# Kernel tuning notes

Hardware: AMD Instinct MI355X
Metric: run time of the kernel (lower is better)

## Reference

```python
import jax, jax.numpy as jnp
import numpy as np

WIN = 7          # window height/width
P = 10           # prompts_len
HEADS = 12
B0 = 32          # image batch (spa_prompts batch)
NW = 64          # windows per image
NW_TOK = WIN * WIN  # 49


def _relative_position_index(w):
    coords = np.stack(np.meshgrid(np.arange(w), np.arange(w), indexing='ij'))  # [2,w,w]
    flat = coords.reshape(2, -1)                        # [2, w*w]
    rel = flat[:, :, None] - flat[:, None, :]           # [2, w*w, w*w]
    rel = rel.transpose(1, 2, 0).astype(np.int64)       # [w*w, w*w, 2]
    rel[..., 0] += w - 1
    rel[..., 1] += w - 1
    rel[..., 0] *= 2 * w - 1
    return rel.sum(-1)                                  # [w*w, w*w]

REL_IDX = jnp.asarray(_relative_position_index(WIN))    # [49,49] int


def setup_inputs() -> dict:
    key = jax.random.key(0)
    ks = jax.random.split(key, 8)
    dim = 384
    return {
        'x': jax.random.normal(ks[0], (B0 * NW, NW_TOK, dim), jnp.float32),
        'spa_prompts': jax.random.normal(ks[1], (B0, P, dim), jnp.float32),
        'mask': jax.random.normal(ks[2], (NW, NW_TOK, NW_TOK), jnp.float32),
        'bias_table': jax.random.normal(ks[3], (169, HEADS), jnp.float32) * 0.02,
        'w_qkv': jax.random.normal(ks[4], (3 * dim, dim), jnp.float32) * 0.02,
        'b_qkv': jax.random.normal(ks[5], (3 * dim,), jnp.float32) * 0.02,
        'w_proj': jax.random.normal(ks[6], (dim, dim), jnp.float32) * 0.02,
        'b_proj': jax.random.normal(ks[7], (dim,), jnp.float32) * 0.02,
    }


def reference(x, spa_prompts, mask, bias_table, w_qkv, b_qkv, w_proj, b_proj):
    B_, Nw, C = x.shape
    b0 = spa_prompts.shape[0]
    nW = B_ // b0
    hd = C // HEADS
    scale = hd ** -0.5

    # broadcast prompts to every window and prepend
    prompts = jnp.broadcast_to(spa_prompts[:, None], (b0, nW, P, C)).reshape(B_, P, C)
    xc = jnp.concatenate([prompts, x], axis=1)          # [B_, N, C], N = P + Nw
    N = xc.shape[1]

    qkv = xc @ w_qkv.T + b_qkv                          # [B_, N, 3C]
    qkv = qkv.reshape(B_, N, 3, HEADS, hd).transpose(2, 0, 3, 1, 4)
    q, k, v = qkv[0], qkv[1], qkv[2]                    # [B_, H, N, hd]

    attn_weight = jnp.einsum('bhnd,bhmd->bhnm', q, k)   # unscaled, returned

    # relative position bias gathered for the window block, padded over prompt rows/cols
    rpb = bias_table[REL_IDX.reshape(-1)].reshape(NW_TOK, NW_TOK, HEADS)
    rpb = rpb.transpose(2, 0, 1)                        # [H, 49, 49]
    bias_full = jnp.pad(rpb, ((0, 0), (P, 0), (P, 0)))  # [H, N, N]

    attn = attn_weight * scale + bias_full[None]

    mask_full = jnp.pad(mask, ((0, 0), (P, 0), (P, 0)))  # [nW, N, N]
    attn = attn.reshape(b0, nW, HEADS, N, N) + mask_full[None, :, None]
    attn = jax.nn.softmax(attn.reshape(B_, HEADS, N, N), axis=-1)

    out = jnp.einsum('bhnm,bhmd->bnhd', attn, v).reshape(B_, N, C)
    out = out @ w_proj.T + b_proj

    prompts_out = out[:, :P].reshape(b0, nW, P, C).mean(axis=1)
    x_out = out[:, P:]
    return (x_out, attn_weight, prompts_out)
```

## Files before the change

kernel.cpp:

```cpp
#include <hip/hip_runtime.h>
#include <hip/hip_bf16.h>

#define P     10
#define NTOK  59
#define HEADS 12
#define NWTOK 49

#define AW_OFF 38535168
#define PO_OFF 124096512

typedef __attribute__((ext_vector_type(8))) short short8;
typedef __attribute__((ext_vector_type(8))) unsigned short ushort8;
typedef __attribute__((ext_vector_type(4))) float floatx4;
typedef float f4u __attribute__((ext_vector_type(4), aligned(4)));
typedef unsigned int uint_g __attribute__((address_space(1)));
typedef unsigned int uint_l __attribute__((address_space(3)));

__device__ __forceinline__ unsigned short f2b(float f) {
  unsigned u = __builtin_bit_cast(unsigned, f);
  u += 0x7fffu + ((u >> 16) & 1u);
  return (unsigned short)(u >> 16);
}

__device__ __forceinline__ void gll16(const void* g, void* l) {
  __builtin_amdgcn_global_load_lds((const uint_g*)g, (uint_l*)l, 16, 0, 0);
}

__global__ __launch_bounds__(256) void convert_w_kernel(
    const float* __restrict__ w, unsigned short* __restrict__ wb) {
  const int i = (blockIdx.x * 256 + threadIdx.x) * 8;
  const float4 a = *(const float4*)(w + i);
  const float4 b = *(const float4*)(w + i + 4);
  ushort8 o;
  o[0] = f2b(a.x); o[1] = f2b(a.y); o[2] = f2b(a.z); o[3] = f2b(a.w);
  o[4] = f2b(b.x); o[5] = f2b(b.y); o[6] = f2b(b.z); o[7] = f2b(b.w);
  *(ushort8*)(wb + i) = o;
}

__global__ __launch_bounds__(256) void combo_kernel(
    const float* __restrict__ mask, const float* __restrict__ bias_table,
    float* __restrict__ combo) {
  const int bid = blockIdx.x;
  const int h = bid % HEADS, wnd = bid / HEADS;
  for (int e = threadIdx.x; e < 2401; e += 256) {
    const int ti = e / 49, tj = e - (e / 49) * 49;
    const int ai = ti / 7, aj = ti - ai * 7;
    const int bi = tj / 7, bj = tj - bi * 7;
    const int ridx = (ai - bi + 6) * 13 + (aj - bj + 6);
    combo[(size_t)bid * 2401 + e] =
        bias_table[ridx * HEADS + h] + mask[(size_t)wnd * 2401 + e];
  }
}

__global__ __launch_bounds__(256) void gemm_qkv_kernel(
    const unsigned short* __restrict__ xb, const unsigned short* __restrict__ xp,
    const unsigned short* __restrict__ Bw, const float* __restrict__ b_qkv,
    unsigned short* __restrict__ qkx, unsigned short* __restrict__ qkp) {
  __shared__ unsigned short Asw[8192];
  __shared__ unsigned short Bsw[8192];
  const int t = threadIdx.x;
  const int w = t >> 6, lane = t & 63;
  const int lr = lane & 15, lg = lane >> 4;
  const int w0 = w >> 1, w1 = w & 1;
  const int by = blockIdx.y;
  const bool isP = by >= 784;
  const int n0 = blockIdx.x * 128;
  const int srow = lane >> 3, cpos = lane & 7;

  floatx4 acc[4][4];
#pragma unroll
  for (int mr = 0; mr < 4; ++mr)
#pragma unroll
    for (int nc = 0; nc < 4; ++nc) acc[mr][nc] = (floatx4)0.f;

  for (int k0 = 0; k0 < 384; k0 += 64) {
#pragma unroll
    for (int i = 0; i < 4; ++i) {
      const int r = (w * 4 + i) * 8 + srow;
      const int c = cpos ^ (r & 7);
      const unsigned short* asrc;
      if (!isP) {
        asrc = xb + (size_t)(by * 128 + r) * 384 + k0 + c * 8;
      } else {
        int mp = (by - 784) * 128 + r;
        if (mp > 319) mp = 319;
        asrc = xp + (size_t)mp * 384 + k0 + c * 8;
      }
      gll16(asrc, Asw + (w * 4 + i) * 512);
      gll16(Bw + (size_t)(n0 + r) * 384 + k0 + c * 8, Bsw + (w * 4 + i) * 512);
    }
    __syncthreads();
#pragma unroll
    for (int kh = 0; kh < 2; ++kh) {
      short8 af[4], bf[4];
#pragma unroll
      for (int mr = 0; mr < 4; ++mr) {
        const int r = w0 * 64 + mr * 16 + lr;
        af[mr] = *(const short8*)(Asw + r * 64 + (((kh * 4 + lg) ^ (r & 7)) * 8));
      }
#pragma unroll
      for (int nc = 0; nc < 4; ++nc) {
        const int r = w1 * 64 + nc * 16 + lr;
        bf[nc] = *(const short8*)(Bsw + r * 64 + (((kh * 4 + lg) ^ (r & 7)) * 8));
      }
#pragma unroll
      for (int mr = 0; mr < 4; ++mr)
#pragma unroll
        for (int nc = 0; nc < 4; ++nc)
          acc[mr][nc] = __builtin_amdgcn_mfma_f32_16x16x32_bf16(
              af[mr], bf[nc], acc[mr][nc], 0, 0, 0);
    }
    __syncthreads();
  }

  const int sec = blockIdx.x / 3;
  float bias[4]; int hh[4], dd[4];
#pragma unroll
  for (int nc = 0; nc < 4; ++nc) {
    const int n = n0 + w1 * 64 + nc * 16 + lr;
    bias[nc] = b_qkv[n];
    hh[nc] = (n >> 5) % 12;
    dd[nc] = n & 31;
  }
#pragma unroll
  for (int mr = 0; mr < 4; ++mr)
#pragma unroll
    for (int reg = 0; reg < 4; ++reg) {
      const int rloc = w0 * 64 + mr * 16 + lg * 4 + reg;
      if (!isP) {
        const int m = by * 128 + rloc;
        const int bb = m / 49, tok = m - bb * 49;
        const size_t base = (size_t)(bb * 3 + sec) * 12 * 1568 + (size_t)tok * 32;
#pragma unroll
        for (int nc = 0; nc < 4; ++nc)
          qkx[base + (size_t)hh[nc] * 1568 + dd[nc]] =
              f2b(acc[mr][nc][reg] + bias[nc]);
      } else {
        const int mp = (by - 784) * 128 + rloc;
        if (mp < 320) {
          const int b0 = mp / 10, ptok = mp - b0 * 10;
          const size_t base = (size_t)(b0 * 3 + sec) * 12 * 320 + (size_t)ptok * 32;
#pragma unroll
          for (int nc = 0; nc < 4; ++nc)
            qkp[base + (size_t)hh[nc] * 320 + dd[nc]] =
                f2b(acc[mr][nc][reg] + bias[nc]);
        }
      }
    }
}

__global__ __launch_bounds__(256) void attn_kernel(
    const unsigned short* __restrict__ qkx, const unsigned short* __restrict__ qkp,
    const float* __restrict__ combo, float* __restrict__ aw_out,
    unsigned short* __restrict__ attn_bf) {
  __shared__ char lds[14976];
  unsigned short* qs = (unsigned short*)(lds);
  unsigned short* ks = (unsigned short*)(lds + 5120);
  unsigned short* vt = (unsigned short*)(lds + 10240);
  unsigned short* Pm = (unsigned short*)(lds);

  const int blk = blockIdx.x;
  const int b = blk / HEADS, h = blk - b * HEADS;
  const int t = threadIdx.x;
  const int w = t >> 6, lane = t & 63, lr = lane & 15, lg = lane >> 4;

  if (t < 236) {
    const int row = t >> 2, dc = (t & 3) * 8;
    ushort8 q8, k8, v8;
    if (row < P) {
      const size_t base =
          ((size_t)((b >> 6) * 3) * 12 + h) * 320 + row * 32 + dc;
      q8 = *(const ushort8*)(qkp + base);
      k8 = *(const ushort8*)(qkp + base + 12 * 320);
      v8 = *(const ushort8*)(qkp + base + 24 * 320);
    } else {
      const size_t base =
          ((size_t)(b * 3) * 12 + h) * 1568 + (row - P) * 32 + dc;
      q8 = *(const ushort8*)(qkx + base);
      k8 = *(const ushort8*)(qkx + base + 12 * 1568);
      v8 = *(const ushort8*)(qkx + base + 24 * 1568);
    }
    *(ushort8*)(qs + row * 40 + dc) = q8;
    *(ushort8*)(ks + row * 40 + dc) = k8;
#pragma unroll
    for (int j = 0; j < 8; ++j) vt[(dc + j) * 74 + row] = v8[j];
  } else {
    const int e = t - 236;
#pragma unroll
    for (int jj = 0; jj < 8; ++jj) {
      const int f = e * 8 + jj;
      vt[(f / 5) * 74 + 59 + (f % 5)] = 0;
    }
  }
  __syncthreads();

  const int q = w * 16 + lr;
  const short8 qa = *(const short8*)(qs + q * 40 + lg * 8);
  floatx4 sacc[4];
#pragma unroll
  for (int nt = 0; nt < 4; ++nt) {
    const short8 kb = *(const short8*)(ks + (nt * 16 + lr) * 40 + lg * 8);
    sacc[nt] = __builtin_amdgcn_mfma_f32_16x16x32_bf16(kb, qa, (floatx4)0.f, 0, 0, 0);
  }

  if (q < NTOK) {
    float* rowp = aw_out + (size_t)blk * 3481 + q * 59;
#pragma unroll
    for (int nt = 0; nt < 3; ++nt)
      *(f4u*)(rowp + nt * 16 + lg * 4) = __builtin_bit_cast(f4u, sacc[nt]);
    if (lg < 2) {
      *(f4u*)(rowp + 48 + lg * 4) = __builtin_bit_cast(f4u, sacc[3]);
    } else if (lg == 2) {
      rowp[56] = sacc[3][0];
      rowp[57] = sacc[3][1];
      rowp[58] = sacc[3][2];
    }
  }

  const float scale = 0.17677669529663687f;
  const float* comb = combo + (size_t)((b & 63) * HEADS + h) * 2401;
  float ev[4][4];
  float mx = -3.0e38f;
#pragma unroll
  for (int nt = 0; nt < 4; ++nt)
#pragma unroll
    for (int reg = 0; reg < 4; ++reg) {
      const int kk = nt * 16 + lg * 4 + reg;
      float v = -3.0e38f;
      if (q < NTOK && kk < NTOK) {
        const float cb = (q >= P && kk >= P) ? comb[(q - P) * 49 + (kk - P)] : 0.f;
        v = fmaf(sacc[nt][reg], scale, cb);
      }
      ev[nt][reg] = v;
      mx = fmaxf(mx, v);
    }
  mx = fmaxf(mx, __shfl_xor(mx, 16));
  mx = fmaxf(mx, __shfl_xor(mx, 32));
  float sm = 0.f;
#pragma unroll
  for (int nt = 0; nt < 4; ++nt)
#pragma unroll
    for (int reg = 0; reg < 4; ++reg) {
      const float e = __expf(ev[nt][reg] - mx);
      ev[nt][reg] = e;
      sm += e;
    }
  sm += __shfl_xor(sm, 16);
  sm += __shfl_xor(sm, 32);
  const float inv = 1.0f / sm;

  __syncthreads();
#pragma unroll
  for (int nt = 0; nt < 4; ++nt) {
    uint2 uu;
    uu.x = (unsigned)f2b(ev[nt][0] * inv) | ((unsigned)f2b(ev[nt][1] * inv) << 16);
    uu.y = (unsigned)f2b(ev[nt][2] * inv) | ((unsigned)f2b(ev[nt][3] * inv) << 16);
    *(uint2*)(Pm + q * 72 + nt * 16 + lg * 4) = uu;
  }

  floatx4 oacc[2];
  oacc[0] = (floatx4)0.f; oacc[1] = (floatx4)0.f;
#pragma unroll
  for (int kk = 0; kk < 2; ++kk) {
    const short8 pa = *(const short8*)(Pm + (w * 16 + lr) * 72 + kk * 32 + lg * 8);
#pragma unroll
    for (int nt = 0; nt < 2; ++nt) {
      const short8 vb = *(const short8*)(vt + (nt * 16 + lr) * 74 + kk * 32 + lg * 8);
      oacc[nt] = __builtin_amdgcn_mfma_f32_16x16x32_bf16(pa, vb, oacc[nt], 0, 0, 0);
    }
  }

  unsigned short* wb = Pm + w * 1152;
#pragma unroll
  for (int nt = 0; nt < 2; ++nt)
#pragma unroll
    for (int reg = 0; reg < 4; ++reg)
      wb[(lg * 4 + reg) * 40 + nt * 16 + lr] = f2b(oacc[nt][reg]);
  const int rr = lane >> 2, c8 = (lane & 3) * 8;
  const int row = w * 16 + rr;
  if (row < NTOK) {
    const ushort8 ov = *(const ushort8*)(wb + rr * 40 + c8);
    *(ushort8*)(attn_bf + ((size_t)(b * NTOK + row)) * 384 + h * 32 + c8) = ov;
  }
}

__global__ __launch_bounds__(256) void gemm_proj_kernel(
    const unsigned short* __restrict__ A, const unsigned short* __restrict__ Bw,
    const float* __restrict__ b_proj, float* __restrict__ x_out,
    float* __restrict__ pbuf) {
  __shared__ unsigned short Asw[8192];
  __shared__ unsigned short Bsw[8192];
  const int t = threadIdx.x;
  const int w = t >> 6, lane = t & 63;
  const int lr = lane & 15, lg = lane >> 4;
  const int w0 = w >> 1, w1 = w & 1;
  const size_t m0 = (size_t)blockIdx.y * 128;
  const int n0 = blockIdx.x * 128;
  const int srow = lane >> 3, cpos = lane & 7;

  floatx4 acc[4][4];
#pragma unroll
  for (int mr = 0; mr < 4; ++mr)
#pragma unroll
    for (int nc = 0; nc < 4; ++nc) acc[mr][nc] = (floatx4)0.f;

  for (int k0 = 0; k0 < 384; k0 += 64) {
#pragma unroll
    for (int i = 0; i < 4; ++i) {
      const int r = (w * 4 + i) * 8 + srow;
      const int c = cpos ^ (r & 7);
      gll16(A + (m0 + r) * 384 + k0 + c * 8, Asw + (w * 4 + i) * 512);
      gll16(Bw + (size_t)(n0 + r) * 384 + k0 + c * 8, Bsw + (w * 4 + i) * 512);
    }
    __syncthreads();
#pragma unroll
    for (int kh = 0; kh < 2; ++kh) {
      short8 af[4], bf[4];
#pragma unroll
      for (int mr = 0; mr < 4; ++mr) {
        const int r = w0 * 64 + mr * 16 + lr;
        af[mr] = *(const short8*)(Asw + r * 64 + (((kh * 4 + lg) ^ (r & 7)) * 8));
      }
#pragma unroll
      for (int nc = 0; nc < 4; ++nc) {
        const int r = w1 * 64 + nc * 16 + lr;
        bf[nc] = *(const short8*)(Bsw + r * 64 + (((kh * 4 + lg) ^ (r & 7)) * 8));
      }
#pragma unroll
      for (int mr = 0; mr < 4; ++mr)
#pragma unroll
        for (int nc = 0; nc < 4; ++nc)
          acc[mr][nc] = __builtin_amdgcn_mfma_f32_16x16x32_bf16(
              af[mr], bf[nc], acc[mr][nc], 0, 0, 0);
    }
    __syncthreads();
  }

  float bias[4]; int nn[4];
#pragma unroll
  for (int nc = 0; nc < 4; ++nc) {
    nn[nc] = n0 + w1 * 64 + nc * 16 + lr;
    bias[nc] = b_proj[nn[nc]];
  }
#pragma unroll
  for (int mr = 0; mr < 4; ++mr)
#pragma unroll
    for (int reg = 0; reg < 4; ++reg) {
      const int m = (int)m0 + w0 * 64 + mr * 16 + lg * 4 + reg;
      const int bb = m / 59, tok = m - bb * 59;
      float* dst = (tok >= P)
          ? x_out + (size_t)(bb * NWTOK + tok - P) * 384
          : pbuf + (size_t)(bb * P + tok) * 384;
#pragma unroll
      for (int nc = 0; nc < 4; ++nc)
        dst[nn[nc]] = acc[mr][nc][reg] + bias[nc];
    }
}

__global__ __launch_bounds__(256) void reduce_prompts_kernel(
    const float* __restrict__ pbuf, float* __restrict__ po) {
  const int o = blockIdx.x * 256 + threadIdx.x;
  const int b0 = o / 3840;
  const int rem = o - b0 * 3840;
  const float* base = pbuf + (size_t)b0 * 64 * 3840 + rem;
  float s = 0.f;
#pragma unroll 8
  for (int w = 0; w < 64; ++w) s += base[(size_t)w * 3840];
  po[o] = s * (1.f / 64.f);
}

extern "C" void kernel_launch(void* const* d_in, const int* in_sizes, int n_in,
                              void* d_out, int out_size, void* d_ws, size_t ws_size,
                              hipStream_t stream) {
  const float* x          = (const float*)d_in[0];
  const float* spa        = (const float*)d_in[1];
  const float* mask       = (const float*)d_in[2];
  const float* bias_table = (const float*)d_in[3];
  const float* w_qkv      = (const float*)d_in[4];
  const float* b_qkv      = (const float*)d_in[5];
  const float* w_proj     = (const float*)d_in[6];
  const float* b_proj     = (const float*)d_in[7];
  float* out = (float*)d_out;

  unsigned short* x_bf     = (unsigned short*)d_ws;
  unsigned short* attn_bf  = (unsigned short*)d_ws;
  unsigned short* xp_bf    = (unsigned short*)((char*)d_ws + 77070336ULL);
  unsigned short* wqkv_bf  = (unsigned short*)((char*)d_ws + 77316096ULL);
  unsigned short* qkx      = (unsigned short*)((char*)d_ws + 92798976ULL);
  unsigned short* qkp      = (unsigned short*)((char*)d_ws + 324009984ULL);
  unsigned short* wproj_bf = (unsigned short*)((char*)d_ws + 324747264ULL);
  float*          pbuf     = (float*)((char*)d_ws + 325042176ULL);
  float*          combo    = (float*)((char*)d_ws + 356499456ULL);

  convert_w_kernel<<<18816, 256, 0, stream>>>(x, x_bf);
  convert_w_kernel<<<60, 256, 0, stream>>>(spa, xp_bf);
  convert_w_kernel<<<216, 256, 0, stream>>>(w_qkv, wqkv_bf);
  convert_w_kernel<<<72, 256, 0, stream>>>(w_proj, wproj_bf);
  combo_kernel<<<768, 256, 0, stream>>>(mask, bias_table, combo);
  gemm_qkv_kernel<<<dim3(9, 787), 256, 0, stream>>>(x_bf, xp_bf, wqkv_bf, b_qkv,
                                                    qkx, qkp);
  attn_kernel<<<2048 * HEADS, 256, 0, stream>>>(qkx, qkp, combo, out + AW_OFF,
                                                attn_bf);
  gemm_proj_kernel<<<dim3(3, 944), 256, 0, stream>>>(attn_bf, wproj_bf, b_proj,
                                                     out, pbuf);
  reduce_prompts_kernel<<<480, 256, 0, stream>>>(pbuf, out + PO_OFF);
}
```

Measured before the change: 594.1 us.

## Stage QKV epilogue through LDS, pad combo bias, swizzle GEMM blocks across XCDs

Three changes in one. The QKV GEMM epilogue now stages bf16 results in LDS and writes contiguous 128-byte rows into a token-major q/k/v layout instead of scattered 2-byte stores, and the attention kernel reads that new layout. The combo bias/mask buffer is padded to 64x64 per head, with zeros in the prompt rows and columns, so the attention kernel can load it with float4 reads and no branch. Both GEMMs also use a 1D grid remapped so that neighbouring tiles land on the same XCD for L2 reuse, at the cost of a larger combo buffer and extra LDS use.

```diff
diff --git a/kernel.cpp b/kernel.cpp
--- a/kernel.cpp
+++ b/kernel.cpp
@@ -24,6 +24,12 @@
 
 __device__ __forceinline__ void gll16(const void* g, void* l) {
   __builtin_amdgcn_global_load_lds((const uint_g*)g, (uint_l*)l, 16, 0, 0);
+}
+
+__device__ __forceinline__ int xcd_swz(int bid, int nwg) {
+  const int q = nwg >> 3, r = nwg & 7;
+  const int xcd = bid & 7, ord = bid >> 3;
+  return (xcd < r ? xcd * (q + 1) : r * (q + 1) + (xcd - r) * q) + ord;
 }
 
 __global__ __launch_bounds__(256) void convert_w_kernel(
@@ -42,13 +48,19 @@
     float* __restrict__ combo) {
   const int bid = blockIdx.x;
   const int h = bid % HEADS, wnd = bid / HEADS;
-  for (int e = threadIdx.x; e < 2401; e += 256) {
-    const int ti = e / 49, tj = e - (e / 49) * 49;
-    const int ai = ti / 7, aj = ti - ai * 7;
-    const int bi = tj / 7, bj = tj - bi * 7;
-    const int ridx = (ai - bi + 6) * 13 + (aj - bj + 6);
-    combo[(size_t)bid * 2401 + e] =
-        bias_table[ridx * HEADS + h] + mask[(size_t)wnd * 2401 + e];
+#pragma unroll
+  for (int e0 = 0; e0 < 4096; e0 += 256) {
+    const int e = e0 + threadIdx.x;
+    const int ti = e >> 6, tj = e & 63;
+    float v = 0.f;
+    if (ti >= P && ti < NTOK && tj >= P && tj < NTOK) {
+      const int a = ti - P, c = tj - P;
+      const int ai = a / 7, aj = a - ai * 7;
+      const int bi = c / 7, bj = c - bi * 7;
+      const int ridx = (ai - bi + 6) * 13 + (aj - bj + 6);
+      v = bias_table[ridx * HEADS + h] + mask[((size_t)wnd * 49 + a) * 49 + c];
+    }
+    combo[((size_t)bid << 12) + e] = v;
   }
 }
 
@@ -56,15 +68,18 @@
     const unsigned short* __restrict__ xb, const unsigned short* __restrict__ xp,
     const unsigned short* __restrict__ Bw, const float* __restrict__ b_qkv,
     unsigned short* __restrict__ qkx, unsigned short* __restrict__ qkp) {
-  __shared__ unsigned short Asw[8192];
-  __shared__ unsigned short Bsw[8192];
+  __shared__ unsigned short sbuf[18432];
+  unsigned short* Asw = sbuf;
+  unsigned short* Bsw = sbuf + 8192;
   const int t = threadIdx.x;
   const int w = t >> 6, lane = t & 63;
   const int lr = lane & 15, lg = lane >> 4;
   const int w0 = w >> 1, w1 = w & 1;
-  const int by = blockIdx.y;
-  const bool isP = by >= 784;
-  const int n0 = blockIdx.x * 128;
+  const int wg = xcd_swz(blockIdx.x, 9 * 787);
+  const int cb = wg % 9;
+  const int my = wg / 9;
+  const bool isP = my >= 784;
+  const int n0 = cb * 128;
   const int srow = lane >> 3, cpos = lane & 7;
 
   floatx4 acc[4][4];
@@ -80,9 +95,9 @@
       const int c = cpos ^ (r & 7);
       const unsigned short* asrc;
       if (!isP) {
-        asrc = xb + (size_t)(by * 128 + r) * 384 + k0 + c * 8;
+        asrc = xb + (size_t)(my * 128 + r) * 384 + k0 + c * 8;
       } else {
-        int mp = (by - 784) * 128 + r;
+        int mp = (my - 784) * 128 + r;
         if (mp > 319) mp = 319;
         asrc = xp + (size_t)mp * 384 + k0 + c * 8;
       }
@@ -113,40 +128,42 @@
     __syncthreads();
   }
 
-  const int sec = blockIdx.x / 3;
-  float bias[4]; int hh[4], dd[4];
-#pragma unroll
-  for (int nc = 0; nc < 4; ++nc) {
-    const int n = n0 + w1 * 64 + nc * 16 + lr;
-    bias[nc] = b_qkv[n];
-    hh[nc] = (n >> 5) % 12;
-    dd[nc] = n & 31;
-  }
+  const int sec = cb / 3;
+  const int nis = (cb - sec * 3) * 128;
+  float bias[4];
+#pragma unroll
+  for (int nc = 0; nc < 4; ++nc)
+    bias[nc] = b_qkv[n0 + w1 * 64 + nc * 16 + lr];
+
+  unsigned short* rp = sbuf + w * 4608;
 #pragma unroll
   for (int mr = 0; mr < 4; ++mr)
 #pragma unroll
-    for (int reg = 0; reg < 4; ++reg) {
-      const int rloc = w0 * 64 + mr * 16 + lg * 4 + reg;
-      if (!isP) {
-        const int m = by * 128 + rloc;
-        const int bb = m / 49, tok = m - bb * 49;
-        const size_t base = (size_t)(bb * 3 + sec) * 12 * 1568 + (size_t)tok * 32;
-#pragma unroll
-        for (int nc = 0; nc < 4; ++nc)
-          qkx[base + (size_t)hh[nc] * 1568 + dd[nc]] =
-              f2b(acc[mr][nc][reg] + bias[nc]);
-      } else {
-        const int mp = (by - 784) * 128 + rloc;
-        if (mp < 320) {
-          const int b0 = mp / 10, ptok = mp - b0 * 10;
-          const size_t base = (size_t)(b0 * 3 + sec) * 12 * 320 + (size_t)ptok * 32;
-#pragma unroll
-          for (int nc = 0; nc < 4; ++nc)
-            qkp[base + (size_t)hh[nc] * 320 + dd[nc]] =
-                f2b(acc[mr][nc][reg] + bias[nc]);
-        }
-      }
-    }
+    for (int nc = 0; nc < 4; ++nc)
+#pragma unroll
+      for (int reg = 0; reg < 4; ++reg)
+        rp[(mr * 16 + lg * 4 + reg) * 72 + nc * 16 + lr] =
+            f2b(acc[mr][nc][reg] + bias[nc]);
+  __syncthreads();
+
+  const int rr = lane;
+  unsigned short* dst = nullptr;
+  if (!isP) {
+    const int m = my * 128 + w0 * 64 + rr;
+    const int bb = m / 49, tok = m - bb * 49;
+    dst = qkx + ((size_t)(bb * 3 + sec) * 49 + tok) * 384 + nis + w1 * 64;
+  } else {
+    const int mp = (my - 784) * 128 + w0 * 64 + rr;
+    if (mp < 320) {
+      const int b0 = mp / 10, ptok = mp - b0 * 10;
+      dst = qkp + ((size_t)(b0 * 3 + sec) * 10 + ptok) * 384 + nis + w1 * 64;
+    }
+  }
+  if (dst) {
+#pragma unroll
+    for (int u = 0; u < 8; ++u)
+      *(ushort8*)(dst + u * 8) = *(const ushort8*)(rp + rr * 72 + u * 8);
+  }
 }
 
 __global__ __launch_bounds__(256) void attn_kernel(
@@ -168,17 +185,17 @@
     const int row = t >> 2, dc = (t & 3) * 8;
     ushort8 q8, k8, v8;
     if (row < P) {
-      const size_t base =
-          ((size_t)((b >> 6) * 3) * 12 + h) * 320 + row * 32 + dc;
-      q8 = *(const ushort8*)(qkp + base);
-      k8 = *(const ushort8*)(qkp + base + 12 * 320);
-      v8 = *(const ushort8*)(qkp + base + 24 * 320);
+      const unsigned short* pb =
+          qkp + ((size_t)((b >> 6) * 3) * 10 + row) * 384 + h * 32 + dc;
+      q8 = *(const ushort8*)(pb);
+      k8 = *(const ushort8*)(pb + 10 * 384);
+      v8 = *(const ushort8*)(pb + 20 * 384);
     } else {
-      const size_t base =
-          ((size_t)(b * 3) * 12 + h) * 1568 + (row - P) * 32 + dc;
-      q8 = *(const ushort8*)(qkx + base);
-      k8 = *(const ushort8*)(qkx + base + 12 * 1568);
-      v8 = *(const ushort8*)(qkx + base + 24 * 1568);
+      const unsigned short* xbp =
+          qkx + ((size_t)(b * 3) * 49 + (row - P)) * 384 + h * 32 + dc;
+      q8 = *(const ushort8*)(xbp);
+      k8 = *(const ushort8*)(xbp + 49 * 384);
+      v8 = *(const ushort8*)(xbp + 98 * 384);
     }
     *(ushort8*)(qs + row * 40 + dc) = q8;
     *(ushort8*)(ks + row * 40 + dc) = k8;
@@ -218,22 +235,23 @@
   }
 
   const float scale = 0.17677669529663687f;
-  const float* comb = combo + (size_t)((b & 63) * HEADS + h) * 2401;
+  const float* comb = combo + (((size_t)((b & 63) * HEADS + h)) << 12) + q * 64;
   float ev[4][4];
   float mx = -3.0e38f;
 #pragma unroll
-  for (int nt = 0; nt < 4; ++nt)
+  for (int nt = 0; nt < 4; ++nt) {
+    const float4 c4 = *(const float4*)(comb + nt * 16 + lg * 4);
+    const float cc[4] = {c4.x, c4.y, c4.z, c4.w};
 #pragma unroll
     for (int reg = 0; reg < 4; ++reg) {
-      const int kk = nt * 16 + lg * 4 + reg;
-      float v = -3.0e38f;
-      if (q < NTOK && kk < NTOK) {
-        const float cb = (q >= P && kk >= P) ? comb[(q - P) * 49 + (kk - P)] : 0.f;
-        v = fmaf(sacc[nt][reg], scale, cb);
-      }
+      const int kk2 = nt * 16 + lg * 4 + reg;
+      const float v = (q < NTOK && kk2 < NTOK)
+                          ? fmaf(sacc[nt][reg], scale, cc[reg])
+                          : -3.0e38f;
       ev[nt][reg] = v;
       mx = fmaxf(mx, v);
     }
+  }
   mx = fmaxf(mx, __shfl_xor(mx, 16));
   mx = fmaxf(mx, __shfl_xor(mx, 32));
   float sm = 0.f;
@@ -294,8 +312,9 @@
   const int w = t >> 6, lane = t & 63;
   const int lr = lane & 15, lg = lane >> 4;
   const int w0 = w >> 1, w1 = w & 1;
-  const size_t m0 = (size_t)blockIdx.y * 128;
-  const int n0 = blockIdx.x * 128;
+  const int wg = xcd_swz(blockIdx.x, 3 * 944);
+  const size_t m0 = (size_t)(wg / 3) * 128;
+  const int n0 = (wg % 3) * 128;
   const int srow = lane >> 3, cpos = lane & 7;
 
   floatx4 acc[4][4];
@@ -397,11 +416,11 @@
   convert_w_kernel<<<216, 256, 0, stream>>>(w_qkv, wqkv_bf);
   convert_w_kernel<<<72, 256, 0, stream>>>(w_proj, wproj_bf);
   combo_kernel<<<768, 256, 0, stream>>>(mask, bias_table, combo);
-  gemm_qkv_kernel<<<dim3(9, 787), 256, 0, stream>>>(x_bf, xp_bf, wqkv_bf, b_qkv,
-                                                    qkx, qkp);
+  gemm_qkv_kernel<<<9 * 787, 256, 0, stream>>>(x_bf, xp_bf, wqkv_bf, b_qkv,
+                                               qkx, qkp);
   attn_kernel<<<2048 * HEADS, 256, 0, stream>>>(qkx, qkp, combo, out + AW_OFF,
                                                 attn_bf);
-  gemm_proj_kernel<<<dim3(3, 944), 256, 0, stream>>>(attn_bf, wproj_bf, b_proj,
-                                                     out, pbuf);
+  gemm_proj_kernel<<<3 * 944, 256, 0, stream>>>(attn_bf, wproj_bf, b_proj,
+                                                out, pbuf);
   reduce_prompts_kernel<<<480, 256, 0, stream>>>(pbuf, out + PO_OFF);
 }
```

Result: no change. 596.4 us (+0.4%).
